# Kernel optimization log

Hardware: AMD Instinct MI355X
Metric: run time of the kernel (lower is better)

Reference implementation:

```python
import jax, jax.numpy as jnp
import numpy as np

HIDDEN = 1024
B, S = 4, 2048


def setup_inputs() -> dict:
    key = jax.random.key(0)
    ks = jax.random.split(key, 8)
    scale = 1.0 / np.sqrt(HIDDEN)
    return {
        "hidden_states": jax.random.normal(ks[0], (B, S, HIDDEN), dtype=jnp.float32),
        "attention_mask": jnp.zeros((B, S, S), dtype=jnp.float32),
        "Wq": jax.random.normal(ks[1], (HIDDEN, HIDDEN), dtype=jnp.float32) * scale,
        "bq": jnp.zeros((HIDDEN,), dtype=jnp.float32),
        "Wk": jax.random.normal(ks[2], (HIDDEN, HIDDEN), dtype=jnp.float32) * scale,
        "bk": jnp.zeros((HIDDEN,), dtype=jnp.float32),
        "Wv": jax.random.normal(ks[3], (HIDDEN, HIDDEN), dtype=jnp.float32) * scale,
        "bv": jnp.zeros((HIDDEN,), dtype=jnp.float32),
    }


def reference(hidden_states, attention_mask, Wq, bq, Wk, bk, Wv, bv):
    # Dense projections (note: no head split in the original module)
    q = jnp.einsum('bsd,de->bse', hidden_states, Wq) + bq  # [B,S,H]
    k = jnp.einsum('bsd,de->bse', hidden_states, Wk) + bk
    v = jnp.einsum('bsd,de->bse', hidden_states, Wv) + bv
    # scores scaled by sqrt(hidden_size) (not per-head dim), per the source
    inv_scale = 1.0 / jnp.sqrt(jnp.asarray(q.shape[-1], dtype=q.dtype))
    scores = jnp.einsum('bqd,bkd->bqk', q, k) * inv_scale  # [B,S,S]
    scores = scores + attention_mask
    weights = jax.nn.softmax(scores, axis=-1)
    # dropout is identity (training=False)
    out = jnp.einsum('bqk,bkd->bqd', weights, v)  # [B,S,H]
    return out
```

## Files before the change

### kernel.cpp

```cpp
#include <hip/hip_runtime.h>
#include <stdint.h>

typedef __attribute__((ext_vector_type(8))) short short8;
typedef __attribute__((ext_vector_type(8))) unsigned short u16x8;
typedef __attribute__((ext_vector_type(4))) float f32x4;

__device__ __forceinline__ uint16_t f2bf(float x) {
  uint32_t u = __float_as_uint(x);
  uint32_t r = (u + 0x7FFFu + ((u >> 16) & 1u)) >> 16;
  return (uint16_t)r;
}
__device__ __forceinline__ float bf2f(uint16_t x) {
  return __uint_as_float(((uint32_t)x) << 16);
}

__device__ __forceinline__ void gl_lds16(const uint16_t* g, void* l) {
  __builtin_amdgcn_global_load_lds(
      (const __attribute__((address_space(1))) void*)g,
      (__attribute__((address_space(3))) void*)l, 16, 0, 0);
}


__global__ __launch_bounds__(256) void cvt_f32_to_bf16(const float* __restrict__ in,
                                                       uint16_t* __restrict__ out) {
  long i = ((long)blockIdx.x * 256 + threadIdx.x) * 8;
  f32x4 v0 = *(const f32x4*)(in + i);
  f32x4 v1 = *(const f32x4*)(in + i + 4);
  u16x8 o;
  o[0] = f2bf(v0[0]); o[1] = f2bf(v0[1]); o[2] = f2bf(v0[2]); o[3] = f2bf(v0[3]);
  o[4] = f2bf(v1[0]); o[5] = f2bf(v1[1]); o[6] = f2bf(v1[2]); o[7] = f2bf(v1[3]);
  *(u16x8*)(out + i) = o;
}

__global__ __launch_bounds__(64) void cvt_w_transpose(const float* __restrict__ W0,
                                                      const float* __restrict__ W1,
                                                      const float* __restrict__ W2,
                                                      uint16_t* __restrict__ WT) {
  const int z = blockIdx.z;
  const float* W = (z == 0) ? W0 : ((z == 1) ? W1 : W2);
  uint16_t* out = WT + (long)z * 1024 * 1024;
  const int n = blockIdx.x * 64 + threadIdx.x;
  const int k0 = blockIdx.y * 128;
  for (int kk = 0; kk < 128; kk += 8) {
    u16x8 o;
#pragma unroll
    for (int j = 0; j < 8; j++) o[j] = f2bf(W[(long)(k0 + kk + j) * 1024 + n]);
    *(u16x8*)(out + (long)n * 1024 + k0 + kk) = o;
  }
}

__global__ __launch_bounds__(256) void transpose_v(const uint16_t* __restrict__ V,
                                                   uint16_t* __restrict__ Vt) {
  __shared__ uint16_t tile[64][66];
  const int b = blockIdx.z;
  const int s0 = blockIdx.x * 64, d0 = blockIdx.y * 64;
  const int t = threadIdx.x;
  const int r = t >> 3, c = (t & 7) * 8;
  const uint16_t* Vb = V + (long)b * 2048 * 1024;
#pragma unroll
  for (int j = 0; j < 2; j++) {
    u16x8 v = *(const u16x8*)(Vb + (long)(s0 + r + 32 * j) * 1024 + d0 + c);
#pragma unroll
    for (int i = 0; i < 8; i++) tile[r + 32 * j][c + i] = v[i];
  }
  __syncthreads();
  uint16_t* Vtb = Vt + (long)b * 1024 * 2048;
#pragma unroll
  for (int j = 0; j < 2; j++) {
    const int d = r + 32 * j;
    u16x8 o;
#pragma unroll
    for (int i = 0; i < 8; i++) o[i] = tile[c + i][d];
    *(u16x8*)(Vtb + (long)(d0 + d) * 2048 + s0 + c) = o;
  }
}

template <int MODE, int AI>
__global__ __launch_bounds__(512, 2) void gemmX(
    const uint16_t* __restrict__ Abase, long sAz,
    const uint16_t* __restrict__ Bbase, long sBz,
    int K, int N,
    char* __restrict__ Cbase, long sCz,
    const float* __restrict__ e0, const float* __restrict__ e1,
    const float* __restrict__ e2,
    const float* __restrict__ maskb, long sMz, float scale,
    float* __restrict__ lsum) {
  constexpr int BM = AI * 32;
  constexpr int ABYTES = BM * 128;
  constexpr int BUFB = ABYTES + 32768;
  __shared__ __align__(16) char lds[2 * BUFB];
  const int t = threadIdx.x;
  const int lane = t & 63;
  const int w = t >> 6;
  const int bm = blockIdx.x, bn = blockIdx.y, bz = blockIdx.z;
  const uint16_t* A = (const uint16_t*)((const char*)Abase + (long)bz * sAz);
  const uint16_t* B = (const uint16_t*)((const char*)Bbase + (long)bz * sBz);

  const int srow = t >> 3;
  const int scol = ((((t & 7) * 16) ^ ((srow & 7) << 4)) >> 1);
  const uint16_t* gA[4];
  const uint16_t* gB[4];
#pragma unroll
  for (int s = 0; s < 4; s++) {
    gA[s] = A + (long)(bm * BM + (s % (AI / 2)) * 64 + srow) * K + scol;
    gB[s] = B + (long)(bn * 256 + s * 64 + srow) * K + scol;
  }

  const int wm = w >> 2, wn = w & 3;
  const int fr = lane & 15, kg = lane >> 4;
  const int X = (fr & 7) << 4;
  const int aRow = (wm * (AI * 16) + fr) * 128 + kg * 16;
  const int bRow = (wn * 64 + fr) * 128 + kg * 16;

  f32x4 acc[AI][4];
#pragma unroll
  for (int i = 0; i < AI; i++)
#pragma unroll
    for (int j = 0; j < 4; j++) acc[i][j] = (f32x4){0.f, 0.f, 0.f, 0.f};

  short8 aR[4][2], bR[4][2];
  const int NT = K >> 6;

#define ARD(off, i, ks) (*(const short8*)(lds + (off) + ((aRow + (i) * 2048 + (ks) * 64) ^ X)))
#define BRD(off, j, ks) (*(const short8*)(lds + ABYTES + (off) + ((bRow + (j) * 2048 + (ks) * 64) ^ X)))
#define STG_A01(off, ko) { gl_lds16(gA[0] + (ko), lds + (off) + w * 1024); \
                           gl_lds16(gA[1] + (ko), lds + (off) + 8192 + w * 1024); }
#define STG_A23(off, ko) { gl_lds16(gA[2] + (ko), lds + (off) + 16384 + w * 1024); \
                           gl_lds16(gA[3] + (ko), lds + (off) + 24576 + w * 1024); }
#define STG_B01(off, ko) { gl_lds16(gB[0] + (ko), lds + ABYTES + (off) + w * 1024); \
                           gl_lds16(gB[1] + (ko), lds + ABYTES + (off) + 8192 + w * 1024); }
#define STG_B23(off, ko) { gl_lds16(gB[2] + (ko), lds + ABYTES + (off) + 16384 + w * 1024); \
                           gl_lds16(gB[3] + (ko), lds + ABYTES + (off) + 24576 + w * 1024); }
#define LGKM0 { asm volatile("s_waitcnt lgkmcnt(0)" ::: "memory"); __builtin_amdgcn_sched_barrier(0); }
#define MFMA16(I0, J0)                                                            \
  __builtin_amdgcn_s_setprio(1);                                                  \
  _Pragma("unroll") for (int i = 0; i < 4; i++)                                   \
  _Pragma("unroll") for (int j = 0; j < 2; j++)                                   \
  _Pragma("unroll") for (int ks = 0; ks < 2; ks++)                                \
    acc[(I0) + i][(J0) + j] = __builtin_amdgcn_mfma_f32_16x16x32_bf16(            \
        aR[i][ks], bR[(J0) + j][ks], acc[(I0) + i][(J0) + j], 0, 0, 0);           \
  __builtin_amdgcn_s_setprio(0);

  if constexpr (AI == 8) { STG_A01(0, 0); STG_A23(0, 0); }
  else                   { STG_A01(0, 0); }
  STG_B01(0, 0); STG_B23(0, 0);

  int curo = 0;
  for (int tt = 0; tt < NT - 1; ++tt) {
    const int nxto = curo ^ BUFB;
    const int ko = (tt + 1) << 6;
    if constexpr (AI == 8) {
      STG_A01(nxto, ko);
      asm volatile("s_waitcnt vmcnt(2)" ::: "memory");
      __builtin_amdgcn_s_barrier();
      __builtin_amdgcn_sched_barrier(0);
#pragma unroll
      for (int i = 0; i < 4; i++) { aR[i][0] = ARD(curo, i, 0); aR[i][1] = ARD(curo, i, 1); }
#pragma unroll
      for (int j = 0; j < 4; j++) { bR[j][0] = BRD(curo, j, 0); bR[j][1] = BRD(curo, j, 1); }
      LGKM0;
      MFMA16(0, 0);
      __builtin_amdgcn_s_barrier();
      STG_A23(nxto, ko);
      __builtin_amdgcn_s_barrier();
      MFMA16(0, 2);
      __builtin_amdgcn_s_barrier();
      STG_B01(nxto, ko);
#pragma unroll
      for (int i = 0; i < 4; i++) { aR[i][0] = ARD(curo, 4 + i, 0); aR[i][1] = ARD(curo, 4 + i, 1); }
      __builtin_amdgcn_s_barrier();
      LGKM0;
      MFMA16(4, 2);
      __builtin_amdgcn_s_barrier();
      STG_B23(nxto, ko);
      __builtin_amdgcn_s_barrier();
      MFMA16(4, 0);
      __builtin_amdgcn_s_barrier();
    } else {
      STG_A01(nxto, ko);
      STG_B01(nxto, ko);
      asm volatile("s_waitcnt vmcnt(4)" ::: "memory");
      __builtin_amdgcn_s_barrier();
      __builtin_amdgcn_sched_barrier(0);
#pragma unroll
      for (int i = 0; i < 4; i++) { aR[i][0] = ARD(curo, i, 0); aR[i][1] = ARD(curo, i, 1); }
#pragma unroll
      for (int j = 0; j < 4; j++) { bR[j][0] = BRD(curo, j, 0); bR[j][1] = BRD(curo, j, 1); }
      LGKM0;
      MFMA16(0, 0);
      __builtin_amdgcn_s_barrier();
      STG_B23(nxto, ko);
      __builtin_amdgcn_s_barrier();
      MFMA16(0, 2);
      __builtin_amdgcn_s_barrier();
    }
    curo = nxto;
  }
  asm volatile("s_waitcnt vmcnt(0)" ::: "memory");
  __builtin_amdgcn_s_barrier();
  __builtin_amdgcn_sched_barrier(0);
#pragma unroll
  for (int i = 0; i < 4; i++) { aR[i][0] = ARD(curo, i, 0); aR[i][1] = ARD(curo, i, 1); }
#pragma unroll
  for (int j = 0; j < 4; j++) { bR[j][0] = BRD(curo, j, 0); bR[j][1] = BRD(curo, j, 1); }
  LGKM0;
  MFMA16(0, 0);
  MFMA16(0, 2);
  if constexpr (AI == 8) {
#pragma unroll
    for (int i = 0; i < 4; i++) { aR[i][0] = ARD(curo, 4 + i, 0); aR[i][1] = ARD(curo, 4 + i, 1); }
    LGKM0;
    MFMA16(4, 2);
    MFMA16(4, 0);
  }

  __syncthreads();
  constexpr int RS = 260;
  float* eL = (float*)lds;
  const int wboff = wm * (16 * RS) + (kg * 4) * RS + wn * 64 + fr;
  const int lr = t >> 4, slab = lr >> 4, row16 = lr & 15, cj = t & 15;
  const float* rb = eL + slab * (16 * RS) + row16 * RS + cj * 16;
  const int grow_base = bm * BM + slab * (AI * 16) + row16;

  f32x4 bias4[4];
  const uint16_t* Cu16 = nullptr;
  float* Cf32 = nullptr;
  uint16_t* Cw = nullptr;
  int colg = 0;
  const float* mk = nullptr;
  if constexpr (MODE == 0) {
    const int zz = bn >> 2;
    const float* bias = (zz == 0) ? e0 : ((zz == 1) ? e1 : e2);
    colg = (bn & 3) * 256 + cj * 16;
#pragma unroll
    for (int q = 0; q < 4; q++) bias4[q] = *(const f32x4*)(bias + colg + q * 4);
    Cw = (uint16_t*)(Cbase + (long)zz * sCz);
  } else if constexpr (MODE == 1) {
    colg = bn * 256 + cj * 16;
    Cw = (uint16_t*)(Cbase + (long)bz * sCz);
    mk = (const float*)((const char*)maskb + (long)bz * sMz);
  } else {
    colg = bn * 256 + cj * 16;
    Cf32 = (float*)(Cbase + (long)bz * sCz);
  }
  (void)Cu16;

#pragma unroll
  for (int i = 0; i < AI; i++) {
#pragma unroll
    for (int j = 0; j < 4; j++)
#pragma unroll
      for (int r = 0; r < 4; r++)
        eL[wboff + r * RS + j * 16] = acc[i][j][r];
    __syncthreads();
    f32x4 v0 = *(const f32x4*)(rb);
    f32x4 v1 = *(const f32x4*)(rb + 4);
    f32x4 v2 = *(const f32x4*)(rb + 8);
    f32x4 v3 = *(const f32x4*)(rb + 12);
    const int grow = grow_base + i * 16;
    if constexpr (MODE == 0) {
      v0 += bias4[0]; v1 += bias4[1]; v2 += bias4[2]; v3 += bias4[3];
      u16x8 o0, o1;
#pragma unroll
      for (int q = 0; q < 4; q++) {
        o0[q] = f2bf(v0[q]); o0[4 + q] = f2bf(v1[q]);
        o1[q] = f2bf(v2[q]); o1[4 + q] = f2bf(v3[q]);
      }
      uint16_t* dst = Cw + (long)grow * 1024 + colg;
      *(u16x8*)dst = o0;
      *(u16x8*)(dst + 8) = o1;
    } else if constexpr (MODE == 1) {
      const float* mrow = mk + (long)grow * N + colg;
      f32x4 m0 = *(const f32x4*)(mrow);
      f32x4 m1 = *(const f32x4*)(mrow + 4);
      f32x4 m2 = *(const f32x4*)(mrow + 8);
      f32x4 m3 = *(const f32x4*)(mrow + 12);
      float e[16];
#pragma unroll
      for (int q = 0; q < 4; q++) {
        e[q] = __expf(v0[q] * scale + m0[q]);
        e[4 + q] = __expf(v1[q] * scale + m1[q]);
        e[8 + q] = __expf(v2[q] * scale + m2[q]);
        e[12 + q] = __expf(v3[q] * scale + m3[q]);
      }
      float ps = 0.f;
#pragma unroll
      for (int q = 0; q < 16; q++) ps += e[q];
      ps += __shfl_xor(ps, 1);
      ps += __shfl_xor(ps, 2);
      ps += __shfl_xor(ps, 4);
      ps += __shfl_xor(ps, 8);
      if ((lane & 15) == 0) atomicAdd(lsum + (long)bz * 2048 + grow, ps);
      u16x8 o0, o1;
#pragma unroll
      for (int q = 0; q < 8; q++) { o0[q] = f2bf(e[q]); o1[q] = f2bf(e[8 + q]); }
      uint16_t* dst = Cw + (long)grow * N + colg;
      *(u16x8*)dst = o0;
      *(u16x8*)(dst + 8) = o1;
    } else {
      const float ri = 1.0f / lsum[(long)bz * 2048 + grow];
      v0 *= ri; v1 *= ri; v2 *= ri; v3 *= ri;
      float* dst = Cf32 + (long)grow * N + colg;
      *(f32x4*)dst = v0;
      *(f32x4*)(dst + 4) = v1;
      *(f32x4*)(dst + 8) = v2;
      *(f32x4*)(dst + 12) = v3;
    }
    __syncthreads();
  }
#undef ARD
#undef BRD
#undef STG_A01
#undef STG_A23
#undef STG_B01
#undef STG_B23
#undef LGKM0
#undef MFMA16
}

extern "C" void kernel_launch(void* const* d_in, const int* in_sizes, int n_in,
                              void* d_out, int out_size, void* d_ws, size_t ws_size,
                              hipStream_t stream) {
  const float* hs = (const float*)d_in[0];
  const float* mask = (const float*)d_in[1];
  const float* Wq = (const float*)d_in[2];
  const float* bq = (const float*)d_in[3];
  const float* Wk = (const float*)d_in[4];
  const float* bk = (const float*)d_in[5];
  const float* Wv = (const float*)d_in[6];
  const float* bv = (const float*)d_in[7];
  float* out = (float*)d_out;

  char* ws = (char*)d_ws;
  uint16_t* hsb = (uint16_t*)ws;
  uint16_t* WT = (uint16_t*)(ws + (16L << 20));
  uint16_t* QKV = (uint16_t*)(ws + (22L << 20));
  uint16_t* Vt = (uint16_t*)(ws + (70L << 20));
  uint16_t* E = (uint16_t*)(ws + (86L << 20));
  float* lsum = (float*)(ws + (118L << 20));

  cvt_f32_to_bf16<<<4096, 256, 0, stream>>>(hs, hsb);
  cvt_w_transpose<<<dim3(16, 8, 3), 64, 0, stream>>>(Wq, Wk, Wv, WT);
  hipMemsetAsync((void*)lsum, 0, 4L * 2048 * sizeof(float), stream);
  gemmX<0, 4><<<dim3(64, 12, 1), 512, 0, stream>>>(
      hsb, 0L, WT, 0L, 1024, 3072, (char*)QKV, 16L << 20,
      bq, bk, bv, nullptr, 0L, 0.f, nullptr);
  transpose_v<<<dim3(32, 16, 4), 256, 0, stream>>>(QKV + 2L * 8192 * 1024, Vt);
  gemmX<1, 8><<<dim3(8, 8, 4), 512, 0, stream>>>(
      QKV, 4L << 20, QKV + 8192L * 1024, 4L << 20, 1024, 2048, (char*)E, 8L << 20,
      nullptr, nullptr, nullptr, mask, 16L << 20, 0.03125f, lsum);
  gemmX<2, 4><<<dim3(16, 4, 4), 512, 0, stream>>>(
      E, 8L << 20, Vt, 4L << 20, 2048, 1024, (char*)out, 8L << 20,
      nullptr, nullptr, nullptr, nullptr, 0L, 0.f, lsum);
}
```

Measured before the change: 194.1 us.

## Triple-buffer LDS stages in AI=4 GEMM path with deeper prefetch

```diff
diff --git a/kernel.cpp b/kernel.cpp
--- a/kernel.cpp
+++ b/kernel.cpp
@@ -88,7 +88,8 @@
   constexpr int BM = AI * 32;
   constexpr int ABYTES = BM * 128;
   constexpr int BUFB = ABYTES + 32768;
-  __shared__ __align__(16) char lds[2 * BUFB];
+  constexpr int NBUF = (AI == 4) ? 3 : 2;
+  __shared__ __align__(16) char lds[NBUF * BUFB];
   const int t = threadIdx.x;
   const int lane = t & 63;
   const int w = t >> 6;
@@ -141,15 +142,12 @@
         aR[i][ks], bR[(J0) + j][ks], acc[(I0) + i][(J0) + j], 0, 0, 0);           \
   __builtin_amdgcn_s_setprio(0);
 
-  if constexpr (AI == 8) { STG_A01(0, 0); STG_A23(0, 0); }
-  else                   { STG_A01(0, 0); }
-  STG_B01(0, 0); STG_B23(0, 0);
-
   int curo = 0;
-  for (int tt = 0; tt < NT - 1; ++tt) {
-    const int nxto = curo ^ BUFB;
-    const int ko = (tt + 1) << 6;
-    if constexpr (AI == 8) {
+  if constexpr (AI == 8) {
+    STG_A01(0, 0); STG_A23(0, 0); STG_B01(0, 0); STG_B23(0, 0);
+    for (int tt = 0; tt < NT - 1; ++tt) {
+      const int nxto = curo ^ BUFB;
+      const int ko = (tt + 1) << 6;
       STG_A01(nxto, ko);
       asm volatile("s_waitcnt vmcnt(2)" ::: "memory");
       __builtin_amdgcn_s_barrier();
@@ -176,42 +174,51 @@
       __builtin_amdgcn_s_barrier();
       MFMA16(4, 0);
       __builtin_amdgcn_s_barrier();
-    } else {
-      STG_A01(nxto, ko);
-      STG_B01(nxto, ko);
-      asm volatile("s_waitcnt vmcnt(4)" ::: "memory");
-      __builtin_amdgcn_s_barrier();
-      __builtin_amdgcn_sched_barrier(0);
-#pragma unroll
-      for (int i = 0; i < 4; i++) { aR[i][0] = ARD(curo, i, 0); aR[i][1] = ARD(curo, i, 1); }
-#pragma unroll
-      for (int j = 0; j < 4; j++) { bR[j][0] = BRD(curo, j, 0); bR[j][1] = BRD(curo, j, 1); }
-      LGKM0;
-      MFMA16(0, 0);
-      __builtin_amdgcn_s_barrier();
-      STG_B23(nxto, ko);
-      __builtin_amdgcn_s_barrier();
-      MFMA16(0, 2);
-      __builtin_amdgcn_s_barrier();
+      curo = nxto;
     }
-    curo = nxto;
-  }
-  asm volatile("s_waitcnt vmcnt(0)" ::: "memory");
-  __builtin_amdgcn_s_barrier();
-  __builtin_amdgcn_sched_barrier(0);
-#pragma unroll
-  for (int i = 0; i < 4; i++) { aR[i][0] = ARD(curo, i, 0); aR[i][1] = ARD(curo, i, 1); }
-#pragma unroll
-  for (int j = 0; j < 4; j++) { bR[j][0] = BRD(curo, j, 0); bR[j][1] = BRD(curo, j, 1); }
-  LGKM0;
-  MFMA16(0, 0);
-  MFMA16(0, 2);
-  if constexpr (AI == 8) {
+    asm volatile("s_waitcnt vmcnt(0)" ::: "memory");
+    __builtin_amdgcn_s_barrier();
+    __builtin_amdgcn_sched_barrier(0);
+#pragma unroll
+    for (int i = 0; i < 4; i++) { aR[i][0] = ARD(curo, i, 0); aR[i][1] = ARD(curo, i, 1); }
+#pragma unroll
+    for (int j = 0; j < 4; j++) { bR[j][0] = BRD(curo, j, 0); bR[j][1] = BRD(curo, j, 1); }
+    LGKM0;
+    MFMA16(0, 0);
+    MFMA16(0, 2);
 #pragma unroll
     for (int i = 0; i < 4; i++) { aR[i][0] = ARD(curo, 4 + i, 0); aR[i][1] = ARD(curo, 4 + i, 1); }
     LGKM0;
     MFMA16(4, 2);
     MFMA16(4, 0);
+  } else {
+    STG_A01(0, 0); STG_B01(0, 0); STG_B23(0, 0);
+    STG_A01(BUFB, 64); STG_B01(BUFB, 64); STG_B23(BUFB, 64);
+    for (int tt = 0; tt < NT; ++tt) {
+      if (tt + 2 < NT) {
+        int b2 = curo + 2 * BUFB;
+        if (b2 >= 3 * BUFB) b2 -= 3 * BUFB;
+        const int ko = (tt + 2) << 6;
+        STG_A01(b2, ko); STG_B01(b2, ko); STG_B23(b2, ko);
+        asm volatile("s_waitcnt vmcnt(12)" ::: "memory");
+      } else if (tt + 1 < NT) {
+        asm volatile("s_waitcnt vmcnt(6)" ::: "memory");
+      } else {
+        asm volatile("s_waitcnt vmcnt(0)" ::: "memory");
+      }
+      __builtin_amdgcn_s_barrier();
+      __builtin_amdgcn_sched_barrier(0);
+#pragma unroll
+      for (int i = 0; i < 4; i++) { aR[i][0] = ARD(curo, i, 0); aR[i][1] = ARD(curo, i, 1); }
+#pragma unroll
+      for (int j = 0; j < 4; j++) { bR[j][0] = BRD(curo, j, 0); bR[j][1] = BRD(curo, j, 1); }
+      LGKM0;
+      MFMA16(0, 0);
+      MFMA16(0, 2);
+      __builtin_amdgcn_s_barrier();
+      curo += BUFB;
+      if (curo >= 3 * BUFB) curo = 0;
+    }
   }
 
   __syncthreads();
@@ -223,7 +230,6 @@
   const int grow_base = bm * BM + slab * (AI * 16) + row16;
 
   f32x4 bias4[4];
-  const uint16_t* Cu16 = nullptr;
   float* Cf32 = nullptr;
   uint16_t* Cw = nullptr;
   int colg = 0;
@@ -243,7 +249,6 @@
     colg = bn * 256 + cj * 16;
     Cf32 = (float*)(Cbase + (long)bz * sCz);
   }
-  (void)Cu16;
 
 #pragma unroll
   for (int i = 0; i < AI; i++) {
```

Measured after the change: 198.2 us. 1.02x slower.

## Use 256x256 tiles everywhere and split-K the PV GEMM with reduction kernel

Applied to the files above, without the earlier changes.

```diff
diff --git a/kernel.cpp b/kernel.cpp
--- a/kernel.cpp
+++ b/kernel.cpp
@@ -75,26 +75,41 @@
   }
 }
 
-template <int MODE, int AI>
+__global__ __launch_bounds__(256) void addnorm(const float* __restrict__ Op,
+                                               const float* __restrict__ lsum,
+                                               float* __restrict__ out) {
+  const long idx = ((long)blockIdx.x * 256 + threadIdx.x) * 4;
+  const int b = (int)(idx >> 21);
+  const long rem = idx & ((1L << 21) - 1);
+  const int q = (int)(rem >> 10);
+  const float ri = 1.0f / lsum[b * 2048 + q];
+  f32x4 v0 = *(const f32x4*)(Op + ((long)(2 * b) << 21) + rem);
+  f32x4 v1 = *(const f32x4*)(Op + ((long)(2 * b + 1) << 21) + rem);
+  f32x4 v = (v0 + v1) * ri;
+  *(f32x4*)(out + idx) = v;
+}
+
+template <int MODE>
 __global__ __launch_bounds__(512, 2) void gemmX(
     const uint16_t* __restrict__ Abase, long sAz,
     const uint16_t* __restrict__ Bbase, long sBz,
-    int K, int N,
+    int K, int Kit, int N,
     char* __restrict__ Cbase, long sCz,
     const float* __restrict__ e0, const float* __restrict__ e1,
     const float* __restrict__ e2,
     const float* __restrict__ maskb, long sMz, float scale,
     float* __restrict__ lsum) {
-  constexpr int BM = AI * 32;
-  constexpr int ABYTES = BM * 128;
-  constexpr int BUFB = ABYTES + 32768;
+  constexpr int ABYTES = 65536 / 2;
+  constexpr int BUFB = 65536;
   __shared__ __align__(16) char lds[2 * BUFB];
   const int t = threadIdx.x;
   const int lane = t & 63;
   const int w = t >> 6;
   const int bm = blockIdx.x, bn = blockIdx.y, bz = blockIdx.z;
-  const uint16_t* A = (const uint16_t*)((const char*)Abase + (long)bz * sAz);
-  const uint16_t* B = (const uint16_t*)((const char*)Bbase + (long)bz * sBz);
+  int bb = bz, koff = 0;
+  if constexpr (MODE == 3) { bb = bz >> 1; koff = (bz & 1) * 1024; }
+  const uint16_t* A = (const uint16_t*)((const char*)Abase + (long)bb * sAz) + koff;
+  const uint16_t* B = (const uint16_t*)((const char*)Bbase + (long)bb * sBz) + koff;
 
   const int srow = t >> 3;
   const int scol = ((((t & 7) * 16) ^ ((srow & 7) << 4)) >> 1);
@@ -102,24 +117,24 @@
   const uint16_t* gB[4];
 #pragma unroll
   for (int s = 0; s < 4; s++) {
-    gA[s] = A + (long)(bm * BM + (s % (AI / 2)) * 64 + srow) * K + scol;
+    gA[s] = A + (long)(bm * 256 + s * 64 + srow) * K + scol;
     gB[s] = B + (long)(bn * 256 + s * 64 + srow) * K + scol;
   }
 
   const int wm = w >> 2, wn = w & 3;
   const int fr = lane & 15, kg = lane >> 4;
   const int X = (fr & 7) << 4;
-  const int aRow = (wm * (AI * 16) + fr) * 128 + kg * 16;
+  const int aRow = (wm * 128 + fr) * 128 + kg * 16;
   const int bRow = (wn * 64 + fr) * 128 + kg * 16;
 
-  f32x4 acc[AI][4];
-#pragma unroll
-  for (int i = 0; i < AI; i++)
+  f32x4 acc[8][4];
+#pragma unroll
+  for (int i = 0; i < 8; i++)
 #pragma unroll
     for (int j = 0; j < 4; j++) acc[i][j] = (f32x4){0.f, 0.f, 0.f, 0.f};
 
   short8 aR[4][2], bR[4][2];
-  const int NT = K >> 6;
+  const int NT = Kit >> 6;
 
 #define ARD(off, i, ks) (*(const short8*)(lds + (off) + ((aRow + (i) * 2048 + (ks) * 64) ^ X)))
 #define BRD(off, j, ks) (*(const short8*)(lds + ABYTES + (off) + ((bRow + (j) * 2048 + (ks) * 64) ^ X)))
@@ -141,59 +156,38 @@
         aR[i][ks], bR[(J0) + j][ks], acc[(I0) + i][(J0) + j], 0, 0, 0);           \
   __builtin_amdgcn_s_setprio(0);
 
-  if constexpr (AI == 8) { STG_A01(0, 0); STG_A23(0, 0); }
-  else                   { STG_A01(0, 0); }
-  STG_B01(0, 0); STG_B23(0, 0);
+  STG_A01(0, 0); STG_A23(0, 0); STG_B01(0, 0); STG_B23(0, 0);
 
   int curo = 0;
   for (int tt = 0; tt < NT - 1; ++tt) {
     const int nxto = curo ^ BUFB;
     const int ko = (tt + 1) << 6;
-    if constexpr (AI == 8) {
-      STG_A01(nxto, ko);
-      asm volatile("s_waitcnt vmcnt(2)" ::: "memory");
-      __builtin_amdgcn_s_barrier();
-      __builtin_amdgcn_sched_barrier(0);
-#pragma unroll
-      for (int i = 0; i < 4; i++) { aR[i][0] = ARD(curo, i, 0); aR[i][1] = ARD(curo, i, 1); }
-#pragma unroll
-      for (int j = 0; j < 4; j++) { bR[j][0] = BRD(curo, j, 0); bR[j][1] = BRD(curo, j, 1); }
-      LGKM0;
-      MFMA16(0, 0);
-      __builtin_amdgcn_s_barrier();
-      STG_A23(nxto, ko);
-      __builtin_amdgcn_s_barrier();
-      MFMA16(0, 2);
-      __builtin_amdgcn_s_barrier();
-      STG_B01(nxto, ko);
-#pragma unroll
-      for (int i = 0; i < 4; i++) { aR[i][0] = ARD(curo, 4 + i, 0); aR[i][1] = ARD(curo, 4 + i, 1); }
-      __builtin_amdgcn_s_barrier();
-      LGKM0;
-      MFMA16(4, 2);
-      __builtin_amdgcn_s_barrier();
-      STG_B23(nxto, ko);
-      __builtin_amdgcn_s_barrier();
-      MFMA16(4, 0);
-      __builtin_amdgcn_s_barrier();
-    } else {
-      STG_A01(nxto, ko);
-      STG_B01(nxto, ko);
-      asm volatile("s_waitcnt vmcnt(4)" ::: "memory");
-      __builtin_amdgcn_s_barrier();
-      __builtin_amdgcn_sched_barrier(0);
-#pragma unroll
-      for (int i = 0; i < 4; i++) { aR[i][0] = ARD(curo, i, 0); aR[i][1] = ARD(curo, i, 1); }
-#pragma unroll
-      for (int j = 0; j < 4; j++) { bR[j][0] = BRD(curo, j, 0); bR[j][1] = BRD(curo, j, 1); }
-      LGKM0;
-      MFMA16(0, 0);
-      __builtin_amdgcn_s_barrier();
-      STG_B23(nxto, ko);
-      __builtin_amdgcn_s_barrier();
-      MFMA16(0, 2);
-      __builtin_amdgcn_s_barrier();
-    }
+    STG_A01(nxto, ko);
+    asm volatile("s_waitcnt vmcnt(2)" ::: "memory");
+    __builtin_amdgcn_s_barrier();
+    __builtin_amdgcn_sched_barrier(0);
+#pragma unroll
+    for (int i = 0; i < 4; i++) { aR[i][0] = ARD(curo, i, 0); aR[i][1] = ARD(curo, i, 1); }
+#pragma unroll
+    for (int j = 0; j < 4; j++) { bR[j][0] = BRD(curo, j, 0); bR[j][1] = BRD(curo, j, 1); }
+    LGKM0;
+    MFMA16(0, 0);
+    __builtin_amdgcn_s_barrier();
+    STG_A23(nxto, ko);
+    __builtin_amdgcn_s_barrier();
+    MFMA16(0, 2);
+    __builtin_amdgcn_s_barrier();
+    STG_B01(nxto, ko);
+#pragma unroll
+    for (int i = 0; i < 4; i++) { aR[i][0] = ARD(curo, 4 + i, 0); aR[i][1] = ARD(curo, 4 + i, 1); }
+    __builtin_amdgcn_s_barrier();
+    LGKM0;
+    MFMA16(4, 2);
+    __builtin_amdgcn_s_barrier();
+    STG_B23(nxto, ko);
+    __builtin_amdgcn_s_barrier();
+    MFMA16(4, 0);
+    __builtin_amdgcn_s_barrier();
     curo = nxto;
   }
   asm volatile("s_waitcnt vmcnt(0)" ::: "memory");
@@ -206,13 +200,11 @@
   LGKM0;
   MFMA16(0, 0);
   MFMA16(0, 2);
-  if constexpr (AI == 8) {
-#pragma unroll
-    for (int i = 0; i < 4; i++) { aR[i][0] = ARD(curo, 4 + i, 0); aR[i][1] = ARD(curo, 4 + i, 1); }
-    LGKM0;
-    MFMA16(4, 2);
-    MFMA16(4, 0);
-  }
+#pragma unroll
+  for (int i = 0; i < 4; i++) { aR[i][0] = ARD(curo, 4 + i, 0); aR[i][1] = ARD(curo, 4 + i, 1); }
+  LGKM0;
+  MFMA16(4, 2);
+  MFMA16(4, 0);
 
   __syncthreads();
   constexpr int RS = 260;
@@ -220,10 +212,9 @@
   const int wboff = wm * (16 * RS) + (kg * 4) * RS + wn * 64 + fr;
   const int lr = t >> 4, slab = lr >> 4, row16 = lr & 15, cj = t & 15;
   const float* rb = eL + slab * (16 * RS) + row16 * RS + cj * 16;
-  const int grow_base = bm * BM + slab * (AI * 16) + row16;
+  const int grow_base = bm * 256 + slab * 128 + row16;
 
   f32x4 bias4[4];
-  const uint16_t* Cu16 = nullptr;
   float* Cf32 = nullptr;
   uint16_t* Cw = nullptr;
   int colg = 0;
@@ -243,10 +234,9 @@
     colg = bn * 256 + cj * 16;
     Cf32 = (float*)(Cbase + (long)bz * sCz);
   }
-  (void)Cu16;
-
-#pragma unroll
-  for (int i = 0; i < AI; i++) {
+
+#pragma unroll
+  for (int i = 0; i < 8; i++) {
 #pragma unroll
     for (int j = 0; j < 4; j++)
 #pragma unroll
@@ -298,8 +288,6 @@
       *(u16x8*)dst = o0;
       *(u16x8*)(dst + 8) = o1;
     } else {
-      const float ri = 1.0f / lsum[(long)bz * 2048 + grow];
-      v0 *= ri; v1 *= ri; v2 *= ri; v3 *= ri;
       float* dst = Cf32 + (long)grow * N + colg;
       *(f32x4*)dst = v0;
       *(f32x4*)(dst + 4) = v1;
@@ -338,18 +326,20 @@
   uint16_t* Vt = (uint16_t*)(ws + (70L << 20));
   uint16_t* E = (uint16_t*)(ws + (86L << 20));
   float* lsum = (float*)(ws + (118L << 20));
+  float* Opart = (float*)ws;
 
   cvt_f32_to_bf16<<<4096, 256, 0, stream>>>(hs, hsb);
   cvt_w_transpose<<<dim3(16, 8, 3), 64, 0, stream>>>(Wq, Wk, Wv, WT);
   hipMemsetAsync((void*)lsum, 0, 4L * 2048 * sizeof(float), stream);
-  gemmX<0, 4><<<dim3(64, 12, 1), 512, 0, stream>>>(
-      hsb, 0L, WT, 0L, 1024, 3072, (char*)QKV, 16L << 20,
+  gemmX<0><<<dim3(32, 12, 1), 512, 0, stream>>>(
+      hsb, 0L, WT, 0L, 1024, 1024, 3072, (char*)QKV, 16L << 20,
       bq, bk, bv, nullptr, 0L, 0.f, nullptr);
   transpose_v<<<dim3(32, 16, 4), 256, 0, stream>>>(QKV + 2L * 8192 * 1024, Vt);
-  gemmX<1, 8><<<dim3(8, 8, 4), 512, 0, stream>>>(
-      QKV, 4L << 20, QKV + 8192L * 1024, 4L << 20, 1024, 2048, (char*)E, 8L << 20,
+  gemmX<1><<<dim3(8, 8, 4), 512, 0, stream>>>(
+      QKV, 4L << 20, QKV + 8192L * 1024, 4L << 20, 1024, 1024, 2048, (char*)E, 8L << 20,
       nullptr, nullptr, nullptr, mask, 16L << 20, 0.03125f, lsum);
-  gemmX<2, 4><<<dim3(16, 4, 4), 512, 0, stream>>>(
-      E, 8L << 20, Vt, 4L << 20, 2048, 1024, (char*)out, 8L << 20,
-      nullptr, nullptr, nullptr, nullptr, 0L, 0.f, lsum);
-}
+  gemmX<3><<<dim3(8, 4, 8), 512, 0, stream>>>(
+      E, 8L << 20, Vt, 4L << 20, 2048, 1024, 1024, (char*)Opart, 2048L * 1024 * 4,
+      nullptr, nullptr, nullptr, nullptr, 0L, 0.f, nullptr);
+  addnorm<<<8192, 256, 0, stream>>>(Opart, lsum, out);
+}
```

Result: slower. 215.6 us (+11.1%).
